# Kernel optimization log

Measured on AMD Instinct MI355X. Metric: run time of the kernel, lower is better.

The kernel has to match this reference:

```python
import jax, jax.numpy as jnp
import numpy as np

H = 1024  # rnn hidden size

def _lstm_layer(x, h0, c0, Wih, Whh, bih, bhh):
    """x: [B,T,F]; returns (ys [B,T,H], hT [B,H], cT [B,H]). Torch gate order i,f,g,o."""
    xs = jnp.swapaxes(x, 0, 1)                       # [T,B,F]
    pre = xs @ Wih.T + (bih + bhh)                   # hoist input GEMM out of scan
    WhhT = Whh.T
    def step(carry, pre_t):
        h, c = carry
        g = pre_t + h @ WhhT                         # [B,4H]
        i, f, gg, o = jnp.split(g, 4, axis=-1)
        c = jax.nn.sigmoid(f) * c + jax.nn.sigmoid(i) * jnp.tanh(gg)
        h = jax.nn.sigmoid(o) * jnp.tanh(c)
        return (h, c), h
    (hT, cT), ys = jax.lax.scan(step, (h0, c0), pre)
    return jnp.swapaxes(ys, 0, 1), hT, cT

def _lstm_stack(x, h0, c0, params):
    """h0,c0: [L,B,H]; params: list of (Wih,Whh,bih,bhh) per layer."""
    hs, cs = [], []
    out = x
    for l, (Wih, Whh, bih, bhh) in enumerate(params):
        out, hT, cT = _lstm_layer(out, h0[l], c0[l], Wih, Whh, bih, bhh)
        hs.append(hT); cs.append(cT)
    return out, jnp.stack(hs), jnp.stack(cs)


def setup_inputs() -> dict:
    key = jax.random.key(0)
    ks = jax.random.split(key, 24)
    B, Tin, F = 128, 256, 8
    Ty = 129
    s = 0.05
    d = {
        'x': jax.random.normal(ks[0], (B, Tin, F), jnp.float32),
        'y': jax.random.normal(ks[1], (B, Ty), jnp.float32),
        # encoder LSTM (2 layers, input 8 -> H)
        'enc_Wih0': s * jax.random.normal(ks[2], (4 * H, F), jnp.float32),
        'enc_Whh0': s * jax.random.normal(ks[3], (4 * H, H), jnp.float32),
        'enc_bih0': s * jax.random.normal(ks[4], (4 * H,), jnp.float32),
        'enc_bhh0': s * jax.random.normal(ks[5], (4 * H,), jnp.float32),
        'enc_Wih1': s * jax.random.normal(ks[6], (4 * H, H), jnp.float32),
        'enc_Whh1': s * jax.random.normal(ks[7], (4 * H, H), jnp.float32),
        'enc_bih1': s * jax.random.normal(ks[8], (4 * H,), jnp.float32),
        'enc_bhh1': s * jax.random.normal(ks[9], (4 * H,), jnp.float32),
        # decoder LSTM (2 layers, input 1 -> H)
        'dec_Wih0': s * jax.random.normal(ks[10], (4 * H, 1), jnp.float32),
        'dec_Whh0': s * jax.random.normal(ks[11], (4 * H, H), jnp.float32),
        'dec_bih0': s * jax.random.normal(ks[12], (4 * H,), jnp.float32),
        'dec_bhh0': s * jax.random.normal(ks[13], (4 * H,), jnp.float32),
        'dec_Wih1': s * jax.random.normal(ks[14], (4 * H, H), jnp.float32),
        'dec_Whh1': s * jax.random.normal(ks[15], (4 * H, H), jnp.float32),
        'dec_bih1': s * jax.random.normal(ks[16], (4 * H,), jnp.float32),
        'dec_bhh1': s * jax.random.normal(ks[17], (4 * H,), jnp.float32),
        # mean / std predictor heads (H -> 1)
        'Wmu': s * jax.random.normal(ks[18], (1, H), jnp.float32),
        'bmu': s * jax.random.normal(ks[19], (1,), jnp.float32),
        'Wsig': s * jax.random.normal(ks[20], (1, H), jnp.float32),
        'bsig': s * jax.random.normal(ks[21], (1,), jnp.float32),
    }
    return d


def reference(x, y,
              enc_Wih0, enc_Whh0, enc_bih0, enc_bhh0,
              enc_Wih1, enc_Whh1, enc_bih1, enc_bhh1,
              dec_Wih0, dec_Whh0, dec_bih0, dec_bhh0,
              dec_Wih1, dec_Whh1, dec_bih1, dec_bhh1,
              Wmu, bmu, Wsig, bsig):
    B = x.shape[0]
    seq_len = y.shape[1] - 1
    L = 2
    h0 = jnp.zeros((L, B, H), x.dtype)
    c0 = jnp.zeros((L, B, H), x.dtype)
    enc_params = [(enc_Wih0, enc_Whh0, enc_bih0, enc_bhh0),
                  (enc_Wih1, enc_Whh1, enc_bih1, enc_bhh1)]
    dec_params = [(dec_Wih0, dec_Whh0, dec_bih0, dec_bhh0),
                  (dec_Wih1, dec_Whh1, dec_bih1, dec_bhh1)]
    _, eh, ec = _lstm_stack(x, h0, c0, enc_params)
    # teacher_forcing = 1.0: decoder inputs are ground-truth y[:, 0:seq_len]
    dec_in = y[:, :seq_len, None]                     # [B,S,1]
    dec_out, _, _ = _lstm_stack(dec_in, eh, ec, dec_params)  # [B,S,H]
    mu = dec_out @ Wmu.T + bmu                        # [B,S,1]
    sigma = jax.nn.softplus(dec_out @ Wsig.T + bsig)  # [B,S,1]
    output_collection = jnp.zeros((B, seq_len, 1), x.dtype)
    return output_collection, mu, sigma
```

## Files before the change

### kernel.cpp

```cpp
#include <hip/hip_runtime.h>
#include <stdint.h>

#define BATCH  128
#define TENC   256
#define TDEC   128
#define NSTEPS 384
#define GP     2176
#define HP     2048
#define HOFF   69632
#define SMEMSZ 135168
#define EXP    65
#define MUSOFF 106496

typedef __attribute__((ext_vector_type(8))) short s16x8;
typedef __attribute__((ext_vector_type(4))) float f32x4;

#define OFF_XBF 0u
#define OFF_YBF 524288u
#define OFF_H0  557056u
#define OFF_H1  1081344u
#define OFF_MU  1605632u
#define OFF_SIG 1671168u
#define OFF_BAR 1736704u
#define WS_END  1738752u

__device__ __forceinline__ unsigned short f2bf(float f) {
  unsigned u = __float_as_uint(f);
  u = u + 0x7fffu + ((u >> 16) & 1u);
  return (unsigned short)(u >> 16);
}
__device__ __forceinline__ float sigm(float x) { return 1.f / (1.f + __expf(-x)); }
__device__ __forceinline__ float tanh_f(float x) {
  float a = fabsf(x);
  float e = __expf(-2.f * a);
  float t = (1.f - e) / (1.f + e);
  return x < 0.f ? -t : t;
}

__device__ __forceinline__ void glds16c(const void* g, void* l) {
  __builtin_amdgcn_global_load_lds((const __attribute__((address_space(1))) void*)g,
                                   (__attribute__((address_space(3))) void*)l, 16, 0, 17);
}
__device__ __forceinline__ unsigned ldcoh(const unsigned* p) {
  unsigned v;
  asm volatile("global_load_dword %0, %1, off sc0 sc1\n\ts_waitcnt vmcnt(0)"
               : "=v"(v) : "v"(p) : "memory");
  return v;
}
__device__ __forceinline__ void stcoh(unsigned* p, unsigned v) {
  asm volatile("global_store_dword %0, %1, off sc0 sc1" :: "v"(p), "v"(v) : "memory");
}
__device__ __forceinline__ void pollcnt(const unsigned* p, unsigned target) {
  for (;;) {
    unsigned v = ldcoh(p);
    if ((int)v >= (int)target) break;
    __builtin_amdgcn_s_sleep(4);
  }
}

#define BARRIER() do { __builtin_amdgcn_s_barrier(); asm volatile("" ::: "memory"); } while (0)
#define WAIT_LGKM() asm volatile("s_waitcnt lgkmcnt(0)" ::: "memory")
#define WAIT_VM()   asm volatile("s_waitcnt vmcnt(0)" ::: "memory")
#define WAIT_BOTH() asm volatile("s_waitcnt vmcnt(0) lgkmcnt(0)" ::: "memory")

__device__ __forceinline__ void load_weights(
    s16x8 (&wfa)[9][4], s16x8 (&wfb)[16][4],
    int w, int u0, int l15, int khi,
    const float* W0h, const float* W0x, int xk,
    const float* W1x, const float* W1h) {
#pragma unroll
  for (int j = 0; j < 9; ++j) {
    int kst = w + 4 * j;
#pragma unroll
    for (int n = 0; n < 4; ++n) {
      int g = n * 1024 + u0 + l15;
      s16x8 v;
#pragma unroll
      for (int e = 0; e < 8; ++e) ((unsigned short*)&v)[e] = 0;
      if (kst < 32) {
        const float* p = W0h + (size_t)g * 1024 + kst * 32 + khi * 8;
#pragma unroll
        for (int e = 0; e < 8; ++e) ((unsigned short*)&v)[e] = f2bf(p[e]);
      } else if (kst == 32) {
        if (khi == 0) {
#pragma unroll
          for (int e = 0; e < 8; ++e)
            if (e < xk) ((unsigned short*)&v)[e] = f2bf(W0x[(size_t)g * xk + e]);
        }
      }
      wfa[j][n] = v;
    }
  }
#pragma unroll
  for (int j = 0; j < 16; ++j) {
    int kst = w + 4 * j;
#pragma unroll
    for (int n = 0; n < 4; ++n) {
      int g = n * 1024 + u0 + l15;
      const float* p = (kst < 32)
          ? (W1x + (size_t)g * 1024 + kst * 32 + khi * 8)
          : (W1h + (size_t)g * 1024 + (kst - 32) * 32 + khi * 8);
      s16x8 v;
#pragma unroll
      for (int e = 0; e < 8; ++e) ((unsigned short*)&v)[e] = f2bf(p[e]);
      wfb[j][n] = v;
    }
  }
}

__global__ void cvt_inputs(const float* __restrict__ x, const float* __restrict__ y,
                           unsigned short* __restrict__ xbf, unsigned short* __restrict__ ybf) {
  int i = blockIdx.x * 256 + threadIdx.x;
  if (i < 262144) xbf[i] = f2bf(x[i]);
  if (i < 16384) {
    int b = i >> 7, t = i & 127;
    ybf[i] = f2bf(y[b * 129 + t]);
  }
}

__global__ void __launch_bounds__(256, 1) lstm_main(
    const float* __restrict__ eWx0, const float* __restrict__ eWh0,
    const float* __restrict__ eB0a, const float* __restrict__ eB0b,
    const float* __restrict__ eWx1, const float* __restrict__ eWh1,
    const float* __restrict__ eB1a, const float* __restrict__ eB1b,
    const float* __restrict__ dWx0, const float* __restrict__ dWh0,
    const float* __restrict__ dB0a, const float* __restrict__ dB0b,
    const float* __restrict__ dWx1, const float* __restrict__ dWh1,
    const float* __restrict__ dB1a, const float* __restrict__ dB1b,
    const float* __restrict__ Wmu, const float* __restrict__ Wsig,
    const unsigned short* __restrict__ xbf, const unsigned short* __restrict__ ybf,
    unsigned short* h0buf, unsigned short* h1buf,
    float* mu_acc, float* sig_acc, unsigned* bars) {
  __shared__ char smem[SMEMSZ];

  const int tid = threadIdx.x;
  const int wg = blockIdx.x;
  const int w = tid >> 6;
  const int lane = tid & 63;
  const int l15 = lane & 15;
  const int khi = lane >> 4;
  const int btile = wg & 3;
  const int utile = wg >> 2;
  const int u0 = utile << 4;
  const int r0 = btile << 5;
  const int key = (l15 & 7) << 4;

  unsigned* cnt1 = bars + btile * 128;
  unsigned* cnt2 = cnt1 + 64;

  const int erow = tid >> 3;
  const int uslot = tid & 7;

  s16x8 wfa[9][4];
  s16x8 wfb[16][4];
  load_weights(wfa, wfb, w, u0, l15, khi, eWh0, eWx0, 8, eWx1, eWh1);

  float b0s[2][4], b1s[2][4];
#pragma unroll
  for (int jj = 0; jj < 2; ++jj) {
    int u = u0 + uslot * 2 + jj;
#pragma unroll
    for (int n = 0; n < 4; ++n) {
      b0s[jj][n] = eB0a[n * 1024 + u] + eB0b[n * 1024 + u];
      b1s[jj][n] = eB1a[n * 1024 + u] + eB1b[n * 1024 + u];
    }
  }
  const float wm0 = Wmu[u0 + uslot * 2], wm1 = Wmu[u0 + uslot * 2 + 1];
  const float wg0 = Wsig[u0 + uslot * 2], wg1 = Wsig[u0 + uslot * 2 + 1];

  float c0a = 0.f, c0b = 0.f, c1a = 0.f, c1b = 0.f;

  {
    s16x8 z;
#pragma unroll
    for (int e = 0; e < 8; ++e) ((unsigned short*)&z)[e] = 0;
    for (int o = tid * 16; o < HOFF; o += 4096) *(s16x8*)(smem + o) = z;
  }
  __syncthreads();

  for (int s = 0; s < NSTEPS; ++s) {
    const int enc = (s < 256) ? 1 : 0;
    const int t = enc ? s : (s - 256);
    const int par = s & 1;

    if (tid < 32) {
      char* wb = smem + tid * GP + 2048;
      s16x8 z;
#pragma unroll
      for (int e = 0; e < 8; ++e) ((unsigned short*)&z)[e] = 0;
#pragma unroll
      for (int q = 0; q < 8; ++q) *(s16x8*)(wb + q * 16) = z;
      int slot = (tid & 7) << 4;
      if (enc) {
        *(s16x8*)(wb + slot) = *(const s16x8*)(xbf + (((size_t)(r0 + tid) * TENC + t) << 3));
      } else {
        s16x8 yv = z;
        ((unsigned short*)&yv)[0] = ybf[(r0 + tid) * TDEC + t];
        *(s16x8*)(wb + slot) = yv;
      }
    }
    if (s == 256) {
      load_weights(wfa, wfb, w, u0, l15, khi, dWh0, dWx0, 1, dWx1, dWh1);
#pragma unroll
      for (int jj = 0; jj < 2; ++jj) {
        int u = u0 + uslot * 2 + jj;
#pragma unroll
        for (int n = 0; n < 4; ++n) {
          b0s[jj][n] = dB0a[n * 1024 + u] + dB0b[n * 1024 + u];
          b1s[jj][n] = dB1a[n * 1024 + u] + dB1b[n * 1024 + u];
        }
      }
    }
    WAIT_LGKM();
    BARRIER();

    f32x4 acc[2][4];
#pragma unroll
    for (int m = 0; m < 2; ++m)
#pragma unroll
      for (int n = 0; n < 4; ++n) acc[m][n] = {0.f, 0.f, 0.f, 0.f};
#pragma unroll
    for (int j = 0; j < 8; ++j) {
      int off = (w + 4 * j) << 6;
#pragma unroll
      for (int m = 0; m < 2; ++m) {
        const s16x8 af = *(const s16x8*)(smem + (m * 16 + l15) * GP + ((off + khi * 16) ^ key));
#pragma unroll
        for (int n = 0; n < 4; ++n)
          acc[m][n] = __builtin_amdgcn_mfma_f32_16x16x32_bf16(af, wfa[j][n], acc[m][n], 0, 0, 0);
      }
    }
    if (w == 0) {
#pragma unroll
      for (int m = 0; m < 2; ++m) {
        const s16x8 af = *(const s16x8*)(smem + (m * 16 + l15) * GP + ((2048 + khi * 16) ^ key));
#pragma unroll
        for (int n = 0; n < 4; ++n)
          acc[m][n] = __builtin_amdgcn_mfma_f32_16x16x32_bf16(af, wfa[8][n], acc[m][n], 0, 0, 0);
      }
    }

    if (w == 3) pollcnt(cnt2, 64u * (unsigned)s);
    BARRIER();
#pragma unroll
    for (int rr = 0; rr < 8; ++rr) {
      int row = w * 8 + rr;
      const char* src = (const char*)(h1buf + (((size_t)par * BATCH + r0 + row) << 10));
      char* dst = smem + HOFF + row * HP;
      glds16c(src + lane * 16, dst);
      glds16c(src + 1024 + lane * 16, dst + 1024);
    }

    WAIT_LGKM();
    BARRIER();
    {
      float* exw = (float*)smem;
#pragma unroll
      for (int m = 0; m < 2; ++m)
#pragma unroll
        for (int n = 0; n < 4; ++n)
#pragma unroll
          for (int r = 0; r < 4; ++r)
            exw[(w * 32 + m * 16 + khi * 4 + r) * EXP + n * 16 + l15] = acc[m][n][r];
    }
    WAIT_LGKM();
    BARRIER();

    {
      const float* exw = (const float*)smem;
      unsigned short* hb = h0buf + (((size_t)(par ^ 1) * BATCH + r0 + erow) << 10);
      float hv[2];
#pragma unroll
      for (int jj = 0; jj < 2; ++jj) {
        int u = uslot * 2 + jj;
        float g[4];
#pragma unroll
        for (int n = 0; n < 4; ++n) {
          int c = n * 16 + u;
          g[n] = exw[erow * EXP + c] + exw[(32 + erow) * EXP + c]
               + exw[(64 + erow) * EXP + c] + exw[(96 + erow) * EXP + c] + b0s[jj][n];
        }
        float cv = jj ? c0b : c0a;
        float cn = sigm(g[1]) * cv + sigm(g[0]) * tanh_f(g[2]);
        if (jj) c0b = cn; else c0a = cn;
        hv[jj] = sigm(g[3]) * tanh_f(cn);
      }
      int uswz = (u0 + uslot * 2) ^ ((erow & 7) << 3);
      unsigned pk = (unsigned)f2bf(hv[0]) | ((unsigned)f2bf(hv[1]) << 16);
      stcoh((unsigned*)(hb + uswz), pk);
    }
    WAIT_VM();
    BARRIER();
    if (tid == 0) atomicAdd(cnt1, 1u);

    f32x4 bcc[2][4];
#pragma unroll
    for (int m = 0; m < 2; ++m)
#pragma unroll
      for (int n = 0; n < 4; ++n) bcc[m][n] = {0.f, 0.f, 0.f, 0.f};
#pragma unroll
    for (int j = 8; j < 12; ++j) {
      int off = (w + 4 * (j - 8)) << 6;
#pragma unroll
      for (int m = 0; m < 2; ++m) {
        const s16x8 af = *(const s16x8*)(smem + HOFF + (m * 16 + l15) * HP + ((off + khi * 16) ^ key));
#pragma unroll
        for (int n = 0; n < 4; ++n)
          bcc[m][n] = __builtin_amdgcn_mfma_f32_16x16x32_bf16(af, wfb[j][n], bcc[m][n], 0, 0, 0);
      }
    }
    if (w == 3) pollcnt(cnt1, 64u * (unsigned)(s + 1));
    BARRIER();
#pragma unroll
    for (int rr = 0; rr < 8; ++rr) {
      int row = w * 8 + rr;
      const char* src = (const char*)(h0buf + (((size_t)(par ^ 1) * BATCH + r0 + row) << 10));
      char* dst = smem + row * GP;
      glds16c(src + lane * 16, dst);
      glds16c(src + 1024 + lane * 16, dst + 1024);
    }
#pragma unroll
    for (int j = 12; j < 16; ++j) {
      int off = (w + 4 * (j - 8)) << 6;
#pragma unroll
      for (int m = 0; m < 2; ++m) {
        const s16x8 af = *(const s16x8*)(smem + HOFF + (m * 16 + l15) * HP + ((off + khi * 16) ^ key));
#pragma unroll
        for (int n = 0; n < 4; ++n)
          bcc[m][n] = __builtin_amdgcn_mfma_f32_16x16x32_bf16(af, wfb[j][n], bcc[m][n], 0, 0, 0);
      }
    }
    WAIT_VM();
    BARRIER();
#pragma unroll
    for (int j = 0; j < 8; ++j) {
      int off = (w + 4 * j) << 6;
#pragma unroll
      for (int m = 0; m < 2; ++m) {
        const s16x8 af = *(const s16x8*)(smem + (m * 16 + l15) * GP + ((off + khi * 16) ^ key));
#pragma unroll
        for (int n = 0; n < 4; ++n)
          bcc[m][n] = __builtin_amdgcn_mfma_f32_16x16x32_bf16(af, wfb[j][n], bcc[m][n], 0, 0, 0);
      }
    }
    WAIT_LGKM();
    BARRIER();
    {
      float* exw = (float*)(smem + HOFF);
#pragma unroll
      for (int m = 0; m < 2; ++m)
#pragma unroll
        for (int n = 0; n < 4; ++n)
#pragma unroll
          for (int r = 0; r < 4; ++r)
            exw[(w * 32 + m * 16 + khi * 4 + r) * EXP + n * 16 + l15] = bcc[m][n][r];
    }
    WAIT_LGKM();
    BARRIER();
    {
      const float* exw = (const float*)(smem + HOFF);
      unsigned short* hb = h1buf + (((size_t)(par ^ 1) * BATCH + r0 + erow) << 10);
      float hv[2];
#pragma unroll
      for (int jj = 0; jj < 2; ++jj) {
        int u = uslot * 2 + jj;
        float g[4];
#pragma unroll
        for (int n = 0; n < 4; ++n) {
          int c = n * 16 + u;
          g[n] = exw[erow * EXP + c] + exw[(32 + erow) * EXP + c]
               + exw[(64 + erow) * EXP + c] + exw[(96 + erow) * EXP + c] + b1s[jj][n];
        }
        float cv = jj ? c1b : c1a;
        float cn = sigm(g[1]) * cv + sigm(g[0]) * tanh_f(g[2]);
        if (jj) c1b = cn; else c1a = cn;
        hv[jj] = sigm(g[3]) * tanh_f(cn);
      }
      int uswz = (u0 + uslot * 2) ^ ((erow & 7) << 3);
      unsigned pk = (unsigned)f2bf(hv[0]) | ((unsigned)f2bf(hv[1]) << 16);
      stcoh((unsigned*)(hb + uswz), pk);
      if (!enc) {
        float* muS = (float*)(smem + MUSOFF);
        muS[uslot * 64 + erow] = hv[0] * wm0 + hv[1] * wm1;
        muS[uslot * 64 + 32 + erow] = hv[0] * wg0 + hv[1] * wg1;
      }
    }
    WAIT_BOTH();
    BARRIER();
    if (tid == 0) atomicAdd(cnt2, 1u);
    if (!enc && tid < 64) {
      const float* muS = (const float*)(smem + MUSOFF);
      float sum = 0.f;
#pragma unroll
      for (int q = 0; q < 8; ++q) sum += muS[q * 64 + tid];
      if (tid < 32) atomicAdd(mu_acc + t * BATCH + r0 + tid, sum);
      else          atomicAdd(sig_acc + t * BATCH + r0 + (tid - 32), sum);
    }
  }
}

__global__ void finalize_k(const float* __restrict__ mu_acc, const float* __restrict__ sig_acc,
                           const float* __restrict__ bmu, const float* __restrict__ bsig,
                           float* __restrict__ out) {
  int i = blockIdx.x * 256 + threadIdx.x;
  if (i >= 16384) return;
  int b = i >> 7, t = i & 127;
  float m = mu_acc[t * 128 + b] + bmu[0];
  float sv = sig_acc[t * 128 + b] + bsig[0];
  float sp = sv > 20.f ? sv : log1pf(__expf(sv));
  out[16384 + i] = m;
  out[32768 + i] = sp;
}

extern "C" void kernel_launch(void* const* d_in, const int* in_sizes, int n_in,
                              void* d_out, int out_size, void* d_ws, size_t ws_size,
                              hipStream_t stream) {
  const float* x    = (const float*)d_in[0];
  const float* y    = (const float*)d_in[1];
  const float* eWx0 = (const float*)d_in[2];
  const float* eWh0 = (const float*)d_in[3];
  const float* eB0a = (const float*)d_in[4];
  const float* eB0b = (const float*)d_in[5];
  const float* eWx1 = (const float*)d_in[6];
  const float* eWh1 = (const float*)d_in[7];
  const float* eB1a = (const float*)d_in[8];
  const float* eB1b = (const float*)d_in[9];
  const float* dWx0 = (const float*)d_in[10];
  const float* dWh0 = (const float*)d_in[11];
  const float* dB0a = (const float*)d_in[12];
  const float* dB0b = (const float*)d_in[13];
  const float* dWx1 = (const float*)d_in[14];
  const float* dWh1 = (const float*)d_in[15];
  const float* dB1a = (const float*)d_in[16];
  const float* dB1b = (const float*)d_in[17];
  const float* Wmu  = (const float*)d_in[18];
  const float* bmu  = (const float*)d_in[19];
  const float* Wsig = (const float*)d_in[20];
  const float* bsig = (const float*)d_in[21];

  char* ws = (char*)d_ws;
  unsigned short* xbf = (unsigned short*)(ws + OFF_XBF);
  unsigned short* ybf = (unsigned short*)(ws + OFF_YBF);
  unsigned short* h0b = (unsigned short*)(ws + OFF_H0);
  unsigned short* h1b = (unsigned short*)(ws + OFF_H1);
  float* mu_acc  = (float*)(ws + OFF_MU);
  float* sig_acc = (float*)(ws + OFF_SIG);
  unsigned* bars = (unsigned*)(ws + OFF_BAR);

  hipMemsetAsync(ws + OFF_H0, 0, WS_END - OFF_H0, stream);
  hipMemsetAsync(d_out, 0, (size_t)16384 * 4, stream);

  cvt_inputs<<<1024, 256, 0, stream>>>(x, y, xbf, ybf);
  lstm_main<<<256, 256, 0, stream>>>(eWx0, eWh0, eB0a, eB0b, eWx1, eWh1, eB1a, eB1b,
                                     dWx0, dWh0, dB0a, dB0b, dWx1, dWh1, dB1a, dB1b,
                                     Wmu, Wsig, xbf, ybf, h0b, h1b, mu_acc, sig_acc, bars);
  finalize_k<<<64, 256, 0, stream>>>(mu_acc, sig_acc, bmu, bsig, (float*)d_out);
}
```

Baseline: 3.898 ms.

## Restructure per-step sync: prefetch next h1 and inputs, per-wave counters, partial-sum projections

Reorganizes the persistent LSTM step loop so the layer-1 hidden-state load and the next step's input staging happen at the end of the previous step, overlapping with the layer-0 MFMA work and dropping several workgroup barriers. Cross-workgroup counters are now incremented once per wave instead of once per block after a barrier. The mu/sigma projection replaces shared-memory staging plus global atomics with shuffle reductions that write per-tile partial sums, which the finalize kernel then reduces. The poll sleep is shortened. Risks are ordering hazards from the removed barriers and extra workspace traffic for the partial sums.

New measurement: 5.857 ms. 50.3% more time.

```diff
diff --git a/kernel.cpp b/kernel.cpp
--- a/kernel.cpp
+++ b/kernel.cpp
@@ -10,7 +10,6 @@
 #define HOFF   69632
 #define SMEMSZ 135168
 #define EXP    65
-#define MUSOFF 106496
 
 typedef __attribute__((ext_vector_type(8))) short s16x8;
 typedef __attribute__((ext_vector_type(4))) float f32x4;
@@ -19,10 +18,10 @@
 #define OFF_YBF 524288u
 #define OFF_H0  557056u
 #define OFF_H1  1081344u
-#define OFF_MU  1605632u
-#define OFF_SIG 1671168u
 #define OFF_BAR 1736704u
 #define WS_END  1738752u
+#define OFF_PMU 2097152u
+#define OFF_PSG 6291456u
 
 __device__ __forceinline__ unsigned short f2bf(float f) {
   unsigned u = __float_as_uint(f);
@@ -54,14 +53,13 @@
   for (;;) {
     unsigned v = ldcoh(p);
     if ((int)v >= (int)target) break;
-    __builtin_amdgcn_s_sleep(4);
+    __builtin_amdgcn_s_sleep(2);
   }
 }
 
 #define BARRIER() do { __builtin_amdgcn_s_barrier(); asm volatile("" ::: "memory"); } while (0)
 #define WAIT_LGKM() asm volatile("s_waitcnt lgkmcnt(0)" ::: "memory")
 #define WAIT_VM()   asm volatile("s_waitcnt vmcnt(0)" ::: "memory")
-#define WAIT_BOTH() asm volatile("s_waitcnt vmcnt(0) lgkmcnt(0)" ::: "memory")
 
 __device__ __forceinline__ void load_weights(
     s16x8 (&wfa)[9][4], s16x8 (&wfb)[16][4],
@@ -130,7 +128,7 @@
     const float* __restrict__ Wmu, const float* __restrict__ Wsig,
     const unsigned short* __restrict__ xbf, const unsigned short* __restrict__ ybf,
     unsigned short* h0buf, unsigned short* h1buf,
-    float* mu_acc, float* sig_acc, unsigned* bars) {
+    float* pmu, float* psg, unsigned* bars) {
   __shared__ char smem[SMEMSZ];
 
   const int tid = threadIdx.x;
@@ -174,31 +172,19 @@
     s16x8 z;
 #pragma unroll
     for (int e = 0; e < 8; ++e) ((unsigned short*)&z)[e] = 0;
-    for (int o = tid * 16; o < HOFF; o += 4096) *(s16x8*)(smem + o) = z;
+    for (int o = tid * 16; o < SMEMSZ; o += 4096) *(s16x8*)(smem + o) = z;
+  }
+  __syncthreads();
+  if (tid < 32) {
+    char* wb = smem + tid * GP + 2048 + ((tid & 7) << 4);
+    *(s16x8*)wb = *(const s16x8*)(xbf + (((size_t)(r0 + tid) * TENC) << 3));
   }
   __syncthreads();
 
   for (int s = 0; s < NSTEPS; ++s) {
     const int enc = (s < 256) ? 1 : 0;
-    const int t = enc ? s : (s - 256);
     const int par = s & 1;
 
-    if (tid < 32) {
-      char* wb = smem + tid * GP + 2048;
-      s16x8 z;
-#pragma unroll
-      for (int e = 0; e < 8; ++e) ((unsigned short*)&z)[e] = 0;
-#pragma unroll
-      for (int q = 0; q < 8; ++q) *(s16x8*)(wb + q * 16) = z;
-      int slot = (tid & 7) << 4;
-      if (enc) {
-        *(s16x8*)(wb + slot) = *(const s16x8*)(xbf + (((size_t)(r0 + tid) * TENC + t) << 3));
-      } else {
-        s16x8 yv = z;
-        ((unsigned short*)&yv)[0] = ybf[(r0 + tid) * TDEC + t];
-        *(s16x8*)(wb + slot) = yv;
-      }
-    }
     if (s == 256) {
       load_weights(wfa, wfb, w, u0, l15, khi, dWh0, dWx0, 1, dWx1, dWh1);
 #pragma unroll
@@ -211,8 +197,6 @@
         }
       }
     }
-    WAIT_LGKM();
-    BARRIER();
 
     f32x4 acc[2][4];
 #pragma unroll
@@ -239,20 +223,9 @@
           acc[m][n] = __builtin_amdgcn_mfma_f32_16x16x32_bf16(af, wfa[8][n], acc[m][n], 0, 0, 0);
       }
     }
-
-    if (w == 3) pollcnt(cnt2, 64u * (unsigned)s);
-    BARRIER();
-#pragma unroll
-    for (int rr = 0; rr < 8; ++rr) {
-      int row = w * 8 + rr;
-      const char* src = (const char*)(h1buf + (((size_t)par * BATCH + r0 + row) << 10));
-      char* dst = smem + HOFF + row * HP;
-      glds16c(src + lane * 16, dst);
-      glds16c(src + 1024 + lane * 16, dst + 1024);
-    }
-
     WAIT_LGKM();
     BARRIER();
+
     {
       float* exw = (float*)smem;
 #pragma unroll
@@ -290,8 +263,8 @@
       stcoh((unsigned*)(hb + uswz), pk);
     }
     WAIT_VM();
-    BARRIER();
-    if (tid == 0) atomicAdd(cnt1, 1u);
+    if ((tid & 63) == 0) atomicAdd(cnt1, 1u);
+    BARRIER();
 
     f32x4 bcc[2][4];
 #pragma unroll
@@ -309,7 +282,24 @@
           bcc[m][n] = __builtin_amdgcn_mfma_f32_16x16x32_bf16(af, wfb[j][n], bcc[m][n], 0, 0, 0);
       }
     }
-    if (w == 3) pollcnt(cnt1, 64u * (unsigned)(s + 1));
+    if (s < NSTEPS - 1 && tid < 32) {
+      char* wb = smem + tid * GP + 2048;
+      s16x8 z;
+#pragma unroll
+      for (int e = 0; e < 8; ++e) ((unsigned short*)&z)[e] = 0;
+#pragma unroll
+      for (int q = 0; q < 8; ++q) *(s16x8*)(wb + q * 16) = z;
+      int slot = (tid & 7) << 4;
+      int s1 = s + 1;
+      if (s1 < 256) {
+        *(s16x8*)(wb + slot) = *(const s16x8*)(xbf + (((size_t)(r0 + tid) * TENC + s1) << 3));
+      } else {
+        s16x8 yv = z;
+        ((unsigned short*)&yv)[0] = ybf[(r0 + tid) * TDEC + (s1 - 256)];
+        *(s16x8*)(wb + slot) = yv;
+      }
+    }
+    if (w == 3) pollcnt(cnt1, 256u * (unsigned)(s + 1));
     BARRIER();
 #pragma unroll
     for (int rr = 0; rr < 8; ++rr) {
@@ -332,6 +322,7 @@
     }
     WAIT_VM();
     BARRIER();
+
 #pragma unroll
     for (int j = 0; j < 8; ++j) {
       int off = (w + 4 * j) << 6;
@@ -343,8 +334,6 @@
           bcc[m][n] = __builtin_amdgcn_mfma_f32_16x16x32_bf16(af, wfb[j][n], bcc[m][n], 0, 0, 0);
       }
     }
-    WAIT_LGKM();
-    BARRIER();
     {
       float* exw = (float*)(smem + HOFF);
 #pragma unroll
@@ -357,6 +346,7 @@
     }
     WAIT_LGKM();
     BARRIER();
+
     {
       const float* exw = (const float*)(smem + HOFF);
       unsigned short* hb = h1buf + (((size_t)(par ^ 1) * BATCH + r0 + erow) << 10);
@@ -380,36 +370,53 @@
       unsigned pk = (unsigned)f2bf(hv[0]) | ((unsigned)f2bf(hv[1]) << 16);
       stcoh((unsigned*)(hb + uswz), pk);
       if (!enc) {
-        float* muS = (float*)(smem + MUSOFF);
-        muS[uslot * 64 + erow] = hv[0] * wm0 + hv[1] * wm1;
-        muS[uslot * 64 + 32 + erow] = hv[0] * wg0 + hv[1] * wg1;
-      }
-    }
-    WAIT_BOTH();
-    BARRIER();
-    if (tid == 0) atomicAdd(cnt2, 1u);
-    if (!enc && tid < 64) {
-      const float* muS = (const float*)(smem + MUSOFF);
-      float sum = 0.f;
-#pragma unroll
-      for (int q = 0; q < 8; ++q) sum += muS[q * 64 + tid];
-      if (tid < 32) atomicAdd(mu_acc + t * BATCH + r0 + tid, sum);
-      else          atomicAdd(sig_acc + t * BATCH + r0 + (tid - 32), sum);
-    }
-  }
-}
-
-__global__ void finalize_k(const float* __restrict__ mu_acc, const float* __restrict__ sig_acc,
+        float sm = hv[0] * wm0 + hv[1] * wm1;
+        float sg = hv[0] * wg0 + hv[1] * wg1;
+#pragma unroll
+        for (int o = 1; o < 8; o <<= 1) { sm += __shfl_xor(sm, o); sg += __shfl_xor(sg, o); }
+        if ((tid & 7) == 0) {
+          size_t idx = (((size_t)(s - 256) * 4 + btile) * 64 + utile) * 32 + erow;
+          pmu[idx] = sm;
+          psg[idx] = sg;
+        }
+      }
+    }
+    WAIT_VM();
+    if ((tid & 63) == 0) atomicAdd(cnt2, 1u);
+    BARRIER();
+
+    if (s < NSTEPS - 1) {
+      if (w == 3) pollcnt(cnt2, 256u * (unsigned)(s + 1));
+      BARRIER();
+#pragma unroll
+      for (int rr = 0; rr < 8; ++rr) {
+        int row = w * 8 + rr;
+        const char* src = (const char*)(h1buf + (((size_t)(par ^ 1) * BATCH + r0 + row) << 10));
+        char* dst = smem + HOFF + row * HP;
+        glds16c(src + lane * 16, dst);
+        glds16c(src + 1024 + lane * 16, dst + 1024);
+      }
+    }
+  }
+}
+
+__global__ void finalize_k(const float* __restrict__ pmu, const float* __restrict__ psg,
                            const float* __restrict__ bmu, const float* __restrict__ bsig,
                            float* __restrict__ out) {
   int i = blockIdx.x * 256 + threadIdx.x;
   if (i >= 16384) return;
-  int b = i >> 7, t = i & 127;
-  float m = mu_acc[t * 128 + b] + bmu[0];
-  float sv = sig_acc[t * 128 + b] + bsig[0];
+  int b = i & 127, t = i >> 7;
+  int bt = b >> 5, er = b & 31;
+  const float* pm = pmu + (((size_t)t * 4 + bt) * 64) * 32 + er;
+  const float* ps = psg + (((size_t)t * 4 + bt) * 64) * 32 + er;
+  float m = 0.f, sv = 0.f;
+#pragma unroll 8
+  for (int u = 0; u < 64; ++u) { m += pm[u * 32]; sv += ps[u * 32]; }
+  m += bmu[0];
+  sv += bsig[0];
   float sp = sv > 20.f ? sv : log1pf(__expf(sv));
-  out[16384 + i] = m;
-  out[32768 + i] = sp;
+  out[16384 + b * 128 + t] = m;
+  out[32768 + b * 128 + t] = sp;
 }
 
 extern "C" void kernel_launch(void* const* d_in, const int* in_sizes, int n_in,
@@ -443,8 +450,8 @@
   unsigned short* ybf = (unsigned short*)(ws + OFF_YBF);
   unsigned short* h0b = (unsigned short*)(ws + OFF_H0);
   unsigned short* h1b = (unsigned short*)(ws + OFF_H1);
-  float* mu_acc  = (float*)(ws + OFF_MU);
-  float* sig_acc = (float*)(ws + OFF_SIG);
+  float* pmu = (float*)(ws + OFF_PMU);
+  float* psg = (float*)(ws + OFF_PSG);
   unsigned* bars = (unsigned*)(ws + OFF_BAR);
 
   hipMemsetAsync(ws + OFF_H0, 0, WS_END - OFF_H0, stream);
@@ -453,6 +460,6 @@
   cvt_inputs<<<1024, 256, 0, stream>>>(x, y, xbf, ybf);
   lstm_main<<<256, 256, 0, stream>>>(eWx0, eWh0, eB0a, eB0b, eWx1, eWh1, eB1a, eB1b,
                                      dWx0, dWh0, dB0a, dB0b, dWx1, dWh1, dB1a, dB1b,
-                                     Wmu, Wsig, xbf, ybf, h0b, h1b, mu_acc, sig_acc, bars);
-  finalize_k<<<64, 256, 0, stream>>>(mu_acc, sig_acc, bmu, bsig, (float*)d_out);
-}
+                                     Wmu, Wsig, xbf, ybf, h0b, h1b, pmu, psg, bars);
+  finalize_k<<<64, 256, 0, stream>>>(pmu, psg, bmu, bsig, (float*)d_out);
+}
```
